# Performance work log

Measured on AMD Instinct MI355X. Metric: run time of the kernel, lower is better.

## Reference

```python
import jax, jax.numpy as jnp
import numpy as np

B, M, N, I, O, NM = 16, 256, 256, 64, 64, 16


def setup_inputs() -> dict:
    key = jax.random.key(0)
    k1, k2, k3, k4, k5 = jax.random.split(key, 5)
    glorot = 1.0 / np.sqrt(I + O)
    return {
        "x": jax.random.normal(k1, (B, M, N, I), dtype=jnp.float32),
        "fw1": jax.random.normal(k2, (I, O, NM, NM, 2), dtype=jnp.float32) * glorot,
        "fw2": jax.random.normal(k3, (I, O, NM, NM, 2), dtype=jnp.float32) * glorot,
        "W": jax.random.normal(k4, (I, O), dtype=jnp.float32) * glorot,
        "b": jnp.zeros((O,), dtype=jnp.float32),
    }


def reference(x, fw1, fw2, W, b):
    # x: [B, M, N, I] -> [B, I, M, N]
    Bs, Ms, Ns, Is = x.shape
    nm = fw1.shape[2]
    xt = jnp.transpose(x, (0, 3, 1, 2))
    # forward rFFT over spatial dims, scaled by 1/sqrt(M*N) as in the TF code
    x_ft = jnp.fft.rfft2(xt, s=(Ms, Ns))  # [B, I, M, N//2+1] complex64
    x_ft = x_ft / jnp.asarray(np.sqrt(Ms * Ns), dtype=x_ft.dtype)
    # complex weights (stack-of-2 real/imag -> complex); complex einsum is
    # exactly the real/imag stacked matmul in the original
    w1 = jax.lax.complex(fw1[..., 0], fw1[..., 1])
    w2 = jax.lax.complex(fw2[..., 0], fw2[..., 1])
    top = jnp.einsum('bixy,ioxy->boxy', x_ft[:, :, :nm, :nm], w1)
    bot = jnp.einsum('bixy,ioxy->boxy', x_ft[:, :, -nm:, :nm], w2)
    mid = jnp.zeros((Bs, top.shape[1], Ms - 2 * nm, nm), dtype=top.dtype)
    out_ft = jnp.concatenate([top, mid, bot], axis=2)          # [B, O, M, nm]
    pad = jnp.zeros((Bs, top.shape[1], Ms, Ms // 2 + 1 - nm), dtype=top.dtype)
    out_ft = jnp.concatenate([out_ft, pad], axis=3)            # [B, O, M, M//2+1]
    y = jnp.fft.irfft2(out_ft, s=(Ns, Ms))                     # [B, O, N, M]
    # TF rescale: sqrt(prod of last two dims of out_ft) = sqrt(N*(M//2+1))
    y = y * jnp.asarray(np.sqrt(Ns * (Ms // 2 + 1)), dtype=y.dtype)
    y = jnp.transpose(y, (0, 2, 3, 1))                         # [B, M, N, O]
    return jax.nn.relu(y @ W + b + y)
```

## Files before the change

### kernel.cpp

```cpp
#include <hip/hip_runtime.h>
#include <hip/hip_bf16.h>


#define PI2F 6.283185307179586f

typedef __attribute__((ext_vector_type(8))) short short8v;
typedef __attribute__((ext_vector_type(4))) float f32x4;

static __device__ __forceinline__ float bf16_to_f(unsigned short h) {
  union { unsigned int u; float f; } v; v.u = ((unsigned int)h) << 16; return v.f;
}
static __device__ __forceinline__ unsigned short f_to_bf16(float f) {
  unsigned int u = __float_as_uint(f);
  u += 0x7fffu + ((u >> 16) & 1u);
  return (unsigned short)(u >> 16);
}

__global__ __launch_bounds__(256) void k_tab(unsigned short* __restrict__ Eg,
                                             unsigned short* __restrict__ CSg) {
  int t = threadIdx.x;
#pragma unroll
  for (int ky = 0; ky < 16; ++ky) {
    int idx = (ky * t) & 255;
    float ss, cc;
    sincosf(PI2F * (float)idx * (1.0f / 256.0f), &ss, &cc);
    Eg[(2 * ky) * 256 + t]     = f_to_bf16(cc);
    Eg[(2 * ky + 1) * 256 + t] = f_to_bf16(-ss);
    CSg[t * 32 + 2 * ky]       = f_to_bf16(cc);
    CSg[t * 32 + 2 * ky + 1]   = f_to_bf16(ss);
  }
}

__global__ __launch_bounds__(256) void k_wt(const float* __restrict__ fw1,
                                            const float* __restrict__ fw2,
                                            float2* __restrict__ wT) {
  int a  = blockIdx.x >> 3;
  int ic = blockIdx.x & 7;
  const float* w = (a < 16) ? fw1 : fw2;
  int xx = a & 15;
#pragma unroll
  for (int k = 0; k < 2; ++k) {
    int p = k * 256 + (int)threadIdx.x;
    int i = ic * 8 + (p >> 6);
    int o = p & 63;
    const float4* s4 = reinterpret_cast<const float4*>(
        w + ((((size_t)i * 64 + o) * 16 + xx) * 16) * 2);
#pragma unroll
    for (int j = 0; j < 8; ++j) {
      float4 q = s4[j];
      wT[(((size_t)(2 * j) * 32 + a) * 64 + i) * 64 + o]     = make_float2(q.x, q.y);
      wT[(((size_t)(2 * j + 1) * 32 + a) * 64 + i) * 64 + o] = make_float2(q.z, q.w);
    }
  }
}

__global__ __launch_bounds__(256) void k1_mfma(const float* __restrict__ x,
                                               const unsigned short* __restrict__ Eg,
                                               float* __restrict__ T) {
  __shared__ unsigned short El[32 * 264];
  int bm = blockIdx.x;
  int b = bm >> 8, m = bm & 255;
  int tid = threadIdx.x;

  {
    const unsigned int* src = reinterpret_cast<const unsigned int*>(Eg);
    unsigned int* dst = reinterpret_cast<unsigned int*>(El);
#pragma unroll
    for (int t = 0; t < 16; ++t) {
      int idx = t * 256 + tid;
      dst[(idx >> 7) * 132 + (idx & 127)] = src[idx];
    }
  }
  __syncthreads();

  int lane = tid & 63, w = tid >> 6;
  int r16 = lane & 15, g4 = lane >> 4;
  const float* xp = x + (size_t)bm * 16384 + (w * 16 + r16);

  f32x4 z = {0.f, 0.f, 0.f, 0.f};
  f32x4 acc0 = z, acc1 = z;

#pragma unroll
  for (int ks = 0; ks < 8; ++ks) {
    int nb = ks * 32 + g4 * 8;
    float xv[8];
#pragma unroll
    for (int j = 0; j < 8; ++j) xv[j] = xp[(size_t)(nb + j) * 64];
    short8v bfr;
#pragma unroll
    for (int j = 0; j < 8; ++j) bfr[j] = (short)f_to_bf16(xv[j]);
    short8v a0 = *reinterpret_cast<const short8v*>(&El[r16 * 264 + nb]);
    short8v a1 = *reinterpret_cast<const short8v*>(&El[(16 + r16) * 264 + nb]);
    acc0 = __builtin_amdgcn_mfma_f32_16x16x32_bf16(a0, bfr, acc0, 0, 0, 0);
    acc1 = __builtin_amdgcn_mfma_f32_16x16x32_bf16(a1, bfr, acc1, 0, 0, 0);
  }

  const float SC = 1.0f / 256.0f;
  int i = w * 16 + r16;
#pragma unroll
  for (int mt = 0; mt < 2; ++mt) {
    f32x4 av = (mt == 0) ? acc0 : acc1;
#pragma unroll
    for (int r = 0; r < 4; ++r) {
      int kc = mt * 16 + g4 * 4 + r;
      int ky = kc >> 1, cmp = kc & 1;
      T[(((size_t)(b * 16 + ky) * 256 + m) * 64 + i) * 2 + cmp] = av[r] * SC;
    }
  }
}

__global__ __launch_bounds__(256) void k2_fwd_m(const float* __restrict__ T,
                                                float* __restrict__ X) {
  int bky = blockIdx.x;
  int ih = threadIdx.x & 15;
  int ag = threadIdx.x >> 4;
  const float* Tp = T + (size_t)bky * 32768 + ih * 8;

  float cd1, sd1n, cd2, sd2n;
  { float ss, cc; sincosf(PI2F * (float)ag * (1.0f / 256.0f), &ss, &cc); cd1 = cc; sd1n = -ss; }
  { float ss, cc; sincosf(PI2F * (float)(ag - 16) * (1.0f / 256.0f), &ss, &cc); cd2 = cc; sd2n = -ss; }
  float c1 = 1.0f, s1 = 0.0f, c2 = 1.0f, s2 = 0.0f;

  float xr1[4], xi1[4], xr2[4], xi2[4];
#pragma unroll
  for (int ii = 0; ii < 4; ++ii) { xr1[ii] = xi1[ii] = xr2[ii] = xi2[ii] = 0.0f; }

#pragma unroll 4
  for (int m = 0; m < 256; ++m) {
    const float4* tp4 = reinterpret_cast<const float4*>(Tp + (size_t)m * 128);
    float4 t0 = tp4[0], t1 = tp4[1];
    float tre[4] = {t0.x, t0.z, t1.x, t1.z};
    float tim[4] = {t0.y, t0.w, t1.y, t1.w};
#pragma unroll
    for (int ii = 0; ii < 4; ++ii) {
      xr1[ii] += tre[ii] * c1 - tim[ii] * s1;
      xi1[ii] += tre[ii] * s1 + tim[ii] * c1;
      xr2[ii] += tre[ii] * c2 - tim[ii] * s2;
      xi2[ii] += tre[ii] * s2 + tim[ii] * c2;
    }
    float cn;
    cn = c1 * cd1 - s1 * sd1n; s1 = c1 * sd1n + s1 * cd1; c1 = cn;
    cn = c2 * cd2 - s2 * sd2n; s2 = c2 * sd2n + s2 * cd2; c2 = cn;
  }

  float* Xp1 = X + ((size_t)bky * 32 + ag) * 128 + ih * 8;
  float* Xp2 = X + ((size_t)bky * 32 + ag + 16) * 128 + ih * 8;
  reinterpret_cast<float4*>(Xp1)[0] = make_float4(xr1[0], xi1[0], xr1[1], xi1[1]);
  reinterpret_cast<float4*>(Xp1)[1] = make_float4(xr1[2], xi1[2], xr1[3], xi1[3]);
  reinterpret_cast<float4*>(Xp2)[0] = make_float4(xr2[0], xi2[0], xr2[1], xi2[1]);
  reinterpret_cast<float4*>(Xp2)[1] = make_float4(xr2[2], xi2[2], xr2[3], xi2[3]);
}

__global__ __launch_bounds__(256) void k3_mix(const float* __restrict__ Xg,
                                              const float* __restrict__ wT,
                                              float* __restrict__ OF) {
  int blk = blockIdx.x;
  int kyy = blk >> 5, a = blk & 31;
  __shared__ float wre[64 * 65];
  __shared__ float wim[64 * 65];
  __shared__ float xsh[16 * 128];

  const float2* wsrc = reinterpret_cast<const float2*>(wT) + (size_t)(kyy * 32 + a) * 4096;
#pragma unroll
  for (int k = 0; k < 16; ++k) {
    int p = k * 256 + (int)threadIdx.x;
    float2 v = wsrc[p];
    int i = p >> 6, o = p & 63;
    wre[i * 65 + o] = v.x;
    wim[i * 65 + o] = v.y;
  }
  {
    int bb = threadIdx.x >> 4, icn = threadIdx.x & 15;
    const float4* xsrc = reinterpret_cast<const float4*>(
        Xg + ((size_t)(bb * 16 + kyy) * 32 + a) * 128);
    float4* xdst = reinterpret_cast<float4*>(xsh + bb * 128);
    xdst[icn * 2]     = xsrc[icn * 2];
    xdst[icn * 2 + 1] = xsrc[icn * 2 + 1];
  }
  __syncthreads();

  int o = threadIdx.x & 63, bg = threadIdx.x >> 6;
#pragma unroll
  for (int bb = 0; bb < 4; ++bb) {
    int b = bg * 4 + bb;
    float ore = 0.0f, oim = 0.0f;
    for (int i = 0; i < 64; ++i) {
      float xr = xsh[b * 128 + 2 * i], xi = xsh[b * 128 + 2 * i + 1];
      float wr = wre[i * 65 + o],     wi = wim[i * 65 + o];
      ore += xr * wr - xi * wi;
      oim += xr * wi + xi * wr;
    }
    reinterpret_cast<float2*>(OF)[(((size_t)b * 16 + kyy) * 32 + a) * 64 + o] =
        make_float2(ore, oim);
  }
}

__global__ __launch_bounds__(256) void k4_inv_kx(const float* __restrict__ OF,
                                                 float* __restrict__ G) {
  int blk = blockIdx.x;
  int b = blk >> 4, ug = blk & 15;
  __shared__ float ofs[16384];
  __shared__ float ct[256], st[256];
  {
    float ssv, ccv;
    sincosf(PI2F * (float)threadIdx.x * (1.0f / 256.0f), &ssv, &ccv);
    ct[threadIdx.x] = ccv;
    st[threadIdx.x] = ssv;
  }
  int o = threadIdx.x & 63, us = threadIdx.x >> 6;
  int u0 = ug * 16 + us * 4;
  const float SC2 = 0.002772904280510622f;

  for (int chunk = 0; chunk < 4; ++chunk) {
    __syncthreads();
    const float4* src = reinterpret_cast<const float4*>(
        OF + (size_t)(b * 16 + chunk * 4) * 4096);
    float4* dst = reinterpret_cast<float4*>(ofs);
#pragma unroll
    for (int k = 0; k < 16; ++k) dst[k * 256 + threadIdx.x] = src[k * 256 + threadIdx.x];
    __syncthreads();

    float accr[4][4], acci[4][4];
#pragma unroll
    for (int du = 0; du < 4; ++du)
#pragma unroll
      for (int kyl = 0; kyl < 4; ++kyl) { accr[du][kyl] = 0.0f; acci[du][kyl] = 0.0f; }

    for (int a = 0; a < 32; ++a) {
      int kx = (a < 16) ? a : (224 + a);
      float ofr[4], ofi[4];
#pragma unroll
      for (int kyl = 0; kyl < 4; ++kyl) {
        ofr[kyl] = ofs[((kyl * 32 + a) * 64 + o) * 2];
        ofi[kyl] = ofs[((kyl * 32 + a) * 64 + o) * 2 + 1];
      }
#pragma unroll
      for (int du = 0; du < 4; ++du) {
        int t = (kx * (u0 + du)) & 255;
        float cv = ct[t], sv = st[t];
#pragma unroll
        for (int kyl = 0; kyl < 4; ++kyl) {
          accr[du][kyl] += ofr[kyl] * cv - ofi[kyl] * sv;
          acci[du][kyl] += ofr[kyl] * sv + ofi[kyl] * cv;
        }
      }
    }
#pragma unroll
    for (int du = 0; du < 4; ++du) {
      int u = u0 + du;
#pragma unroll
      for (int kyl = 0; kyl < 4; ++kyl) {
        int ky = chunk * 4 + kyl;
        float sc = SC2 * ((ky == 0) ? 1.0f : 2.0f);
        reinterpret_cast<float2*>(G)[(((size_t)b * 256 + u) * 16 + ky) * 64 + o] =
            make_float2(accr[du][kyl] * sc, acci[du][kyl] * sc);
      }
    }
  }
}

__global__ __launch_bounds__(256) void k5_mfma(const float* __restrict__ G,
                                               const unsigned short* __restrict__ CSg,
                                               const float* __restrict__ Wg,
                                               const float* __restrict__ bias,
                                               float* __restrict__ out) {
  __shared__ unsigned short csl[256 * 40];
  __shared__ unsigned short gml[64 * 40];
  __shared__ unsigned short yl[256 * 72];
  __shared__ unsigned short wtl[64 * 72];
  __shared__ float bl[64];

  int blk = blockIdx.x;
  int b = blk >> 8, u = blk & 255;
  int tid = threadIdx.x;

  {
    const unsigned int* src = reinterpret_cast<const unsigned int*>(CSg);
    unsigned int* dst = reinterpret_cast<unsigned int*>(csl);
#pragma unroll
    for (int t = 0; t < 16; ++t) {
      int idx = t * 256 + tid;
      dst[(idx >> 4) * 20 + (idx & 15)] = src[idx];
    }
  }
  {
#pragma unroll
    for (int t = 0; t < 16; ++t) {
      int p = t * 256 + tid;
      wtl[(p & 63) * 72 + (p >> 6)] = f_to_bf16(Wg[p]);
    }
  }
  {
    int o = tid & 63, kq = tid >> 6;
    const float2* G2 = reinterpret_cast<const float2*>(G) + ((size_t)blk * 16) * 64;
    unsigned int* gd = reinterpret_cast<unsigned int*>(gml);
#pragma unroll
    for (int q = 0; q < 4; ++q) {
      int ky = kq * 4 + q;
      float2 gv = G2[ky * 64 + o];
      gd[o * 20 + ky] = (unsigned int)f_to_bf16(gv.x) |
                        ((unsigned int)f_to_bf16(-gv.y) << 16);
    }
  }
  if (tid < 64) bl[tid] = bias[tid];
  __syncthreads();

  int lane = tid & 63, w = tid >> 6;
  int r16 = lane & 15, g4 = lane >> 4;
  int kc0 = g4 * 8;

  f32x4 z = {0.f, 0.f, 0.f, 0.f};
  f32x4 acc[4][4];

  short8v af[4], bfx[4];
#pragma unroll
  for (int vt = 0; vt < 4; ++vt)
    af[vt] = *reinterpret_cast<const short8v*>(&csl[(w * 64 + vt * 16 + r16) * 40 + kc0]);
#pragma unroll
  for (int ot = 0; ot < 4; ++ot)
    bfx[ot] = *reinterpret_cast<const short8v*>(&gml[(ot * 16 + r16) * 40 + kc0]);
#pragma unroll
  for (int vt = 0; vt < 4; ++vt)
#pragma unroll
    for (int ot = 0; ot < 4; ++ot)
      acc[vt][ot] = __builtin_amdgcn_mfma_f32_16x16x32_bf16(af[vt], bfx[ot], z, 0, 0, 0);

#pragma unroll
  for (int vt = 0; vt < 4; ++vt)
#pragma unroll
    for (int ot = 0; ot < 4; ++ot)
#pragma unroll
      for (int r = 0; r < 4; ++r)
        yl[(w * 64 + vt * 16 + g4 * 4 + r) * 72 + ot * 16 + r16] = f_to_bf16(acc[vt][ot][r]);
  __syncthreads();

  float bv[4];
#pragma unroll
  for (int ot = 0; ot < 4; ++ot) bv[ot] = bl[ot * 16 + r16];
#pragma unroll
  for (int vt = 0; vt < 4; ++vt)
#pragma unroll
    for (int ot = 0; ot < 4; ++ot)
#pragma unroll
      for (int r = 0; r < 4; ++r) acc[vt][ot][r] += bv[ot];

#pragma unroll
  for (int ks = 0; ks < 2; ++ks) {
    int k0 = ks * 32 + kc0;
    short8v ya[4], wb[4];
#pragma unroll
    for (int vt = 0; vt < 4; ++vt)
      ya[vt] = *reinterpret_cast<const short8v*>(&yl[(w * 64 + vt * 16 + r16) * 72 + k0]);
#pragma unroll
    for (int ot = 0; ot < 4; ++ot)
      wb[ot] = *reinterpret_cast<const short8v*>(&wtl[(ot * 16 + r16) * 72 + k0]);
#pragma unroll
    for (int vt = 0; vt < 4; ++vt)
#pragma unroll
      for (int ot = 0; ot < 4; ++ot)
        acc[vt][ot] = __builtin_amdgcn_mfma_f32_16x16x32_bf16(ya[vt], wb[ot], acc[vt][ot], 0, 0, 0);
  }

  float* ob = out + (size_t)blk * 16384;
#pragma unroll
  for (int vt = 0; vt < 4; ++vt)
#pragma unroll
    for (int r = 0; r < 4; ++r) {
      int v = w * 64 + vt * 16 + g4 * 4 + r;
      float* op = ob + (size_t)v * 64 + r16;
#pragma unroll
      for (int ot = 0; ot < 4; ++ot)
        op[ot * 16] = fmaxf(acc[vt][ot][r], 0.0f);
    }
}

extern "C" void kernel_launch(void* const* d_in, const int* in_sizes, int n_in,
                              void* d_out, int out_size, void* d_ws, size_t ws_size,
                              hipStream_t stream) {
  const float* x   = (const float*)d_in[0];
  const float* fw1 = (const float*)d_in[1];
  const float* fw2 = (const float*)d_in[2];
  const float* W   = (const float*)d_in[3];
  const float* bb  = (const float*)d_in[4];
  float* out = (float*)d_out;

  float* ws = (float*)d_ws;
  float* wT = ws;
  float* T  = ws + 4194304;
  float* X  = ws + 12582912;
  float* OF = ws + 13631488;
  float* G  = T;
  unsigned short* Eg  = (unsigned short*)(ws + 14680064);
  unsigned short* CSg = Eg + 8192;

  hipLaunchKernelGGL(k_tab,    dim3(1),    dim3(256), 0, stream, Eg, CSg);
  hipLaunchKernelGGL(k_wt,     dim3(256),  dim3(256), 0, stream, fw1, fw2, (float2*)wT);
  hipLaunchKernelGGL(k1_mfma,  dim3(4096), dim3(256), 0, stream, x, Eg, T);
  hipLaunchKernelGGL(k2_fwd_m, dim3(256),  dim3(256), 0, stream, T, X);
  hipLaunchKernelGGL(k3_mix,   dim3(512),  dim3(256), 0, stream, X, wT, OF);
  hipLaunchKernelGGL(k4_inv_kx,dim3(256),  dim3(256), 0, stream, OF, G);
  hipLaunchKernelGGL(k5_mfma,  dim3(4096), dim3(256), 0, stream, G, CSg, W, bb, out);
}
```

Measured before the change: 256.6 us.

## Store spectral intermediates in bf16, split DFT stages over more blocks, drop k5 staging

The first-stage output T is now stored as packed bf16 pairs, halving that traffic. The m-direction DFT in k2 is split into four partial chunks, each starting its twiddle at the chunk offset, and k3 sums the partials. k4 is split per ky-chunk across four times as many blocks and writes G already in bf16 MFMA-ready layout. k5 then reads its operands (G, CS table, and a W transpose precomputed in k_tab) directly from global memory instead of staging them in LDS. This exposes more parallelism and cuts bytes moved, at the cost of extra partial-sum traffic and lower-precision intermediates.

After: 241.2 us. -6.0%, faster.

```diff
diff --git a/kernel.cpp b/kernel.cpp
--- a/kernel.cpp
+++ b/kernel.cpp
@@ -15,9 +15,14 @@
   u += 0x7fffu + ((u >> 16) & 1u);
   return (unsigned short)(u >> 16);
 }
+static __device__ __forceinline__ unsigned int pack_bf16(float lo, float hi) {
+  return (unsigned int)f_to_bf16(lo) | ((unsigned int)f_to_bf16(hi) << 16);
+}
 
 __global__ __launch_bounds__(256) void k_tab(unsigned short* __restrict__ Eg,
-                                             unsigned short* __restrict__ CSg) {
+                                             unsigned short* __restrict__ CSg,
+                                             const float* __restrict__ Wg,
+                                             unsigned short* __restrict__ Wtb) {
   int t = threadIdx.x;
 #pragma unroll
   for (int ky = 0; ky < 16; ++ky) {
@@ -29,6 +34,11 @@
     CSg[t * 32 + 2 * ky]       = f_to_bf16(cc);
     CSg[t * 32 + 2 * ky + 1]   = f_to_bf16(ss);
   }
+#pragma unroll
+  for (int k = 0; k < 16; ++k) {
+    int p = k * 256 + t;
+    Wtb[(p & 63) * 64 + (p >> 6)] = f_to_bf16(Wg[p]);
+  }
 }
 
 __global__ __launch_bounds__(256) void k_wt(const float* __restrict__ fw1,
@@ -56,7 +66,7 @@
 
 __global__ __launch_bounds__(256) void k1_mfma(const float* __restrict__ x,
                                                const unsigned short* __restrict__ Eg,
-                                               float* __restrict__ T) {
+                                               unsigned int* __restrict__ Tb) {
   __shared__ unsigned short El[32 * 264];
   int bm = blockIdx.x;
   int b = bm >> 8, m = bm & 255;
@@ -100,37 +110,42 @@
 #pragma unroll
   for (int mt = 0; mt < 2; ++mt) {
     f32x4 av = (mt == 0) ? acc0 : acc1;
-#pragma unroll
-    for (int r = 0; r < 4; ++r) {
-      int kc = mt * 16 + g4 * 4 + r;
-      int ky = kc >> 1, cmp = kc & 1;
-      T[(((size_t)(b * 16 + ky) * 256 + m) * 64 + i) * 2 + cmp] = av[r] * SC;
-    }
-  }
-}
-
-__global__ __launch_bounds__(256) void k2_fwd_m(const float* __restrict__ T,
-                                                float* __restrict__ X) {
-  int bky = blockIdx.x;
+    int ky_a = mt * 8 + g4 * 2;
+    Tb[((size_t)(b * 16 + ky_a) * 256 + m) * 64 + i]       = pack_bf16(av[0] * SC, av[1] * SC);
+    Tb[((size_t)(b * 16 + ky_a + 1) * 256 + m) * 64 + i]   = pack_bf16(av[2] * SC, av[3] * SC);
+  }
+}
+
+__global__ __launch_bounds__(256) void k2_fwd_m(const unsigned int* __restrict__ Tb,
+                                                float* __restrict__ Xp) {
+  int bx = blockIdx.x;
+  int bky = bx & 255, mc = bx >> 8;
+  int m0 = mc * 64;
   int ih = threadIdx.x & 15;
   int ag = threadIdx.x >> 4;
-  const float* Tp = T + (size_t)bky * 32768 + ih * 8;
+  const uint4* Tp4 = reinterpret_cast<const uint4*>(Tb) + (size_t)bky * 4096 + ih;
 
   float cd1, sd1n, cd2, sd2n;
   { float ss, cc; sincosf(PI2F * (float)ag * (1.0f / 256.0f), &ss, &cc); cd1 = cc; sd1n = -ss; }
   { float ss, cc; sincosf(PI2F * (float)(ag - 16) * (1.0f / 256.0f), &ss, &cc); cd2 = cc; sd2n = -ss; }
-  float c1 = 1.0f, s1 = 0.0f, c2 = 1.0f, s2 = 0.0f;
+  float c1, s1, c2, s2;
+  { int t = (ag * m0) & 255; float ss, cc; sincosf(PI2F * (float)t * (1.0f / 256.0f), &ss, &cc); c1 = cc; s1 = -ss; }
+  { int t = ((ag + 240) * m0) & 255; float ss, cc; sincosf(PI2F * (float)t * (1.0f / 256.0f), &ss, &cc); c2 = cc; s2 = -ss; }
 
   float xr1[4], xi1[4], xr2[4], xi2[4];
 #pragma unroll
   for (int ii = 0; ii < 4; ++ii) { xr1[ii] = xi1[ii] = xr2[ii] = xi2[ii] = 0.0f; }
 
 #pragma unroll 4
-  for (int m = 0; m < 256; ++m) {
-    const float4* tp4 = reinterpret_cast<const float4*>(Tp + (size_t)m * 128);
-    float4 t0 = tp4[0], t1 = tp4[1];
-    float tre[4] = {t0.x, t0.z, t1.x, t1.z};
-    float tim[4] = {t0.y, t0.w, t1.y, t1.w};
+  for (int m = 0; m < 64; ++m) {
+    uint4 q = Tp4[(size_t)(m0 + m) * 16];
+    unsigned int dv[4] = {q.x, q.y, q.z, q.w};
+    float tre[4], tim[4];
+#pragma unroll
+    for (int ii = 0; ii < 4; ++ii) {
+      tre[ii] = __uint_as_float(dv[ii] << 16);
+      tim[ii] = __uint_as_float(dv[ii] & 0xffff0000u);
+    }
 #pragma unroll
     for (int ii = 0; ii < 4; ++ii) {
       xr1[ii] += tre[ii] * c1 - tim[ii] * s1;
@@ -143,15 +158,16 @@
     cn = c2 * cd2 - s2 * sd2n; s2 = c2 * sd2n + s2 * cd2; c2 = cn;
   }
 
-  float* Xp1 = X + ((size_t)bky * 32 + ag) * 128 + ih * 8;
-  float* Xp2 = X + ((size_t)bky * 32 + ag + 16) * 128 + ih * 8;
+  float* Xb = Xp + (size_t)mc * 1048576;
+  float* Xp1 = Xb + ((size_t)bky * 32 + ag) * 128 + ih * 8;
+  float* Xp2 = Xb + ((size_t)bky * 32 + ag + 16) * 128 + ih * 8;
   reinterpret_cast<float4*>(Xp1)[0] = make_float4(xr1[0], xi1[0], xr1[1], xi1[1]);
   reinterpret_cast<float4*>(Xp1)[1] = make_float4(xr1[2], xi1[2], xr1[3], xi1[3]);
   reinterpret_cast<float4*>(Xp2)[0] = make_float4(xr2[0], xi2[0], xr2[1], xi2[1]);
   reinterpret_cast<float4*>(Xp2)[1] = make_float4(xr2[2], xi2[2], xr2[3], xi2[3]);
 }
 
-__global__ __launch_bounds__(256) void k3_mix(const float* __restrict__ Xg,
+__global__ __launch_bounds__(256) void k3_mix(const float* __restrict__ Xp,
                                               const float* __restrict__ wT,
                                               float* __restrict__ OF) {
   int blk = blockIdx.x;
@@ -171,11 +187,18 @@
   }
   {
     int bb = threadIdx.x >> 4, icn = threadIdx.x & 15;
-    const float4* xsrc = reinterpret_cast<const float4*>(
-        Xg + ((size_t)(bb * 16 + kyy) * 32 + a) * 128);
+    size_t off = ((size_t)(bb * 16 + kyy) * 32 + a) * 128;
+    float4 a0 = make_float4(0.f, 0.f, 0.f, 0.f), a1 = a0;
+#pragma unroll
+    for (int c = 0; c < 4; ++c) {
+      const float4* xsrc = reinterpret_cast<const float4*>(Xp + (size_t)c * 1048576 + off);
+      float4 q0 = xsrc[icn * 2], q1 = xsrc[icn * 2 + 1];
+      a0.x += q0.x; a0.y += q0.y; a0.z += q0.z; a0.w += q0.w;
+      a1.x += q1.x; a1.y += q1.y; a1.z += q1.z; a1.w += q1.w;
+    }
     float4* xdst = reinterpret_cast<float4*>(xsh + bb * 128);
-    xdst[icn * 2]     = xsrc[icn * 2];
-    xdst[icn * 2 + 1] = xsrc[icn * 2 + 1];
+    xdst[icn * 2]     = a0;
+    xdst[icn * 2 + 1] = a1;
   }
   __syncthreads();
 
@@ -196,9 +219,9 @@
 }
 
 __global__ __launch_bounds__(256) void k4_inv_kx(const float* __restrict__ OF,
-                                                 float* __restrict__ G) {
-  int blk = blockIdx.x;
-  int b = blk >> 4, ug = blk & 15;
+                                                 uint4* __restrict__ Gb4) {
+  int bx = blockIdx.x;
+  int b = bx >> 6, ug = (bx >> 2) & 15, chunk = bx & 3;
   __shared__ float ofs[16384];
   __shared__ float ct[256], st[256];
   {
@@ -207,104 +230,68 @@
     ct[threadIdx.x] = ccv;
     st[threadIdx.x] = ssv;
   }
+  {
+    const float4* src = reinterpret_cast<const float4*>(
+        OF + ((size_t)b * 16 + chunk * 4) * 4096);
+    float4* dst = reinterpret_cast<float4*>(ofs);
+#pragma unroll
+    for (int k = 0; k < 16; ++k) dst[k * 256 + threadIdx.x] = src[k * 256 + threadIdx.x];
+  }
+  __syncthreads();
+
   int o = threadIdx.x & 63, us = threadIdx.x >> 6;
   int u0 = ug * 16 + us * 4;
   const float SC2 = 0.002772904280510622f;
 
-  for (int chunk = 0; chunk < 4; ++chunk) {
-    __syncthreads();
-    const float4* src = reinterpret_cast<const float4*>(
-        OF + (size_t)(b * 16 + chunk * 4) * 4096);
-    float4* dst = reinterpret_cast<float4*>(ofs);
-#pragma unroll
-    for (int k = 0; k < 16; ++k) dst[k * 256 + threadIdx.x] = src[k * 256 + threadIdx.x];
-    __syncthreads();
-
-    float accr[4][4], acci[4][4];
-#pragma unroll
-    for (int du = 0; du < 4; ++du)
-#pragma unroll
-      for (int kyl = 0; kyl < 4; ++kyl) { accr[du][kyl] = 0.0f; acci[du][kyl] = 0.0f; }
-
-    for (int a = 0; a < 32; ++a) {
-      int kx = (a < 16) ? a : (224 + a);
-      float ofr[4], ofi[4];
+  float accr[4][4], acci[4][4];
+#pragma unroll
+  for (int du = 0; du < 4; ++du)
+#pragma unroll
+    for (int kyl = 0; kyl < 4; ++kyl) { accr[du][kyl] = 0.0f; acci[du][kyl] = 0.0f; }
+
+  for (int a = 0; a < 32; ++a) {
+    int kx = (a < 16) ? a : (224 + a);
+    float ofr[4], ofi[4];
+#pragma unroll
+    for (int kyl = 0; kyl < 4; ++kyl) {
+      ofr[kyl] = ofs[((kyl * 32 + a) * 64 + o) * 2];
+      ofi[kyl] = ofs[((kyl * 32 + a) * 64 + o) * 2 + 1];
+    }
+#pragma unroll
+    for (int du = 0; du < 4; ++du) {
+      int t = (kx * (u0 + du)) & 255;
+      float cv = ct[t], sv = st[t];
 #pragma unroll
       for (int kyl = 0; kyl < 4; ++kyl) {
-        ofr[kyl] = ofs[((kyl * 32 + a) * 64 + o) * 2];
-        ofi[kyl] = ofs[((kyl * 32 + a) * 64 + o) * 2 + 1];
+        accr[du][kyl] += ofr[kyl] * cv - ofi[kyl] * sv;
+        acci[du][kyl] += ofr[kyl] * sv + ofi[kyl] * cv;
       }
-#pragma unroll
-      for (int du = 0; du < 4; ++du) {
-        int t = (kx * (u0 + du)) & 255;
-        float cv = ct[t], sv = st[t];
-#pragma unroll
-        for (int kyl = 0; kyl < 4; ++kyl) {
-          accr[du][kyl] += ofr[kyl] * cv - ofi[kyl] * sv;
-          acci[du][kyl] += ofr[kyl] * sv + ofi[kyl] * cv;
-        }
-      }
-    }
-#pragma unroll
-    for (int du = 0; du < 4; ++du) {
-      int u = u0 + du;
-#pragma unroll
-      for (int kyl = 0; kyl < 4; ++kyl) {
-        int ky = chunk * 4 + kyl;
-        float sc = SC2 * ((ky == 0) ? 1.0f : 2.0f);
-        reinterpret_cast<float2*>(G)[(((size_t)b * 256 + u) * 16 + ky) * 64 + o] =
-            make_float2(accr[du][kyl] * sc, acci[du][kyl] * sc);
-      }
-    }
-  }
-}
-
-__global__ __launch_bounds__(256) void k5_mfma(const float* __restrict__ G,
+    }
+  }
+#pragma unroll
+  for (int du = 0; du < 4; ++du) {
+    int u = u0 + du;
+    unsigned int wv[4];
+#pragma unroll
+    for (int kyl = 0; kyl < 4; ++kyl) {
+      int ky = chunk * 4 + kyl;
+      float sc = SC2 * ((ky == 0) ? 1.0f : 2.0f);
+      wv[kyl] = pack_bf16(accr[du][kyl] * sc, -acci[du][kyl] * sc);
+    }
+    uint4 pk; pk.x = wv[0]; pk.y = wv[1]; pk.z = wv[2]; pk.w = wv[3];
+    Gb4[(((size_t)b * 256 + u) * 64 + o) * 4 + chunk] = pk;
+  }
+}
+
+__global__ __launch_bounds__(256) void k5_mfma(const unsigned short* __restrict__ Gb,
                                                const unsigned short* __restrict__ CSg,
-                                               const float* __restrict__ Wg,
+                                               const unsigned short* __restrict__ Wtb,
                                                const float* __restrict__ bias,
                                                float* __restrict__ out) {
-  __shared__ unsigned short csl[256 * 40];
-  __shared__ unsigned short gml[64 * 40];
   __shared__ unsigned short yl[256 * 72];
-  __shared__ unsigned short wtl[64 * 72];
-  __shared__ float bl[64];
 
   int blk = blockIdx.x;
-  int b = blk >> 8, u = blk & 255;
   int tid = threadIdx.x;
-
-  {
-    const unsigned int* src = reinterpret_cast<const unsigned int*>(CSg);
-    unsigned int* dst = reinterpret_cast<unsigned int*>(csl);
-#pragma unroll
-    for (int t = 0; t < 16; ++t) {
-      int idx = t * 256 + tid;
-      dst[(idx >> 4) * 20 + (idx & 15)] = src[idx];
-    }
-  }
-  {
-#pragma unroll
-    for (int t = 0; t < 16; ++t) {
-      int p = t * 256 + tid;
-      wtl[(p & 63) * 72 + (p >> 6)] = f_to_bf16(Wg[p]);
-    }
-  }
-  {
-    int o = tid & 63, kq = tid >> 6;
-    const float2* G2 = reinterpret_cast<const float2*>(G) + ((size_t)blk * 16) * 64;
-    unsigned int* gd = reinterpret_cast<unsigned int*>(gml);
-#pragma unroll
-    for (int q = 0; q < 4; ++q) {
-      int ky = kq * 4 + q;
-      float2 gv = G2[ky * 64 + o];
-      gd[o * 20 + ky] = (unsigned int)f_to_bf16(gv.x) |
-                        ((unsigned int)f_to_bf16(-gv.y) << 16);
-    }
-  }
-  if (tid < 64) bl[tid] = bias[tid];
-  __syncthreads();
-
   int lane = tid & 63, w = tid >> 6;
   int r16 = lane & 15, g4 = lane >> 4;
   int kc0 = g4 * 8;
@@ -315,10 +302,11 @@
   short8v af[4], bfx[4];
 #pragma unroll
   for (int vt = 0; vt < 4; ++vt)
-    af[vt] = *reinterpret_cast<const short8v*>(&csl[(w * 64 + vt * 16 + r16) * 40 + kc0]);
+    af[vt] = *reinterpret_cast<const short8v*>(&CSg[(w * 64 + vt * 16 + r16) * 32 + kc0]);
 #pragma unroll
   for (int ot = 0; ot < 4; ++ot)
-    bfx[ot] = *reinterpret_cast<const short8v*>(&gml[(ot * 16 + r16) * 40 + kc0]);
+    bfx[ot] = *reinterpret_cast<const short8v*>(
+        &Gb[((size_t)blk * 64 + ot * 16 + r16) * 32 + kc0]);
 #pragma unroll
   for (int vt = 0; vt < 4; ++vt)
 #pragma unroll
@@ -334,15 +322,14 @@
         yl[(w * 64 + vt * 16 + g4 * 4 + r) * 72 + ot * 16 + r16] = f_to_bf16(acc[vt][ot][r]);
   __syncthreads();
 
-  float bv[4];
-#pragma unroll
-  for (int ot = 0; ot < 4; ++ot) bv[ot] = bl[ot * 16 + r16];
-#pragma unroll
-  for (int vt = 0; vt < 4; ++vt)
-#pragma unroll
-    for (int ot = 0; ot < 4; ++ot)
-#pragma unroll
-      for (int r = 0; r < 4; ++r) acc[vt][ot][r] += bv[ot];
+#pragma unroll
+  for (int ot = 0; ot < 4; ++ot) {
+    float bv = bias[ot * 16 + r16];
+#pragma unroll
+    for (int vt = 0; vt < 4; ++vt)
+#pragma unroll
+      for (int r = 0; r < 4; ++r) acc[vt][ot][r] += bv;
+  }
 
 #pragma unroll
   for (int ks = 0; ks < 2; ++ks) {
@@ -353,7 +340,7 @@
       ya[vt] = *reinterpret_cast<const short8v*>(&yl[(w * 64 + vt * 16 + r16) * 72 + k0]);
 #pragma unroll
     for (int ot = 0; ot < 4; ++ot)
-      wb[ot] = *reinterpret_cast<const short8v*>(&wtl[(ot * 16 + r16) * 72 + k0]);
+      wb[ot] = *reinterpret_cast<const short8v*>(&Wtb[(ot * 16 + r16) * 64 + k0]);
 #pragma unroll
     for (int vt = 0; vt < 4; ++vt)
 #pragma unroll
@@ -385,19 +372,21 @@
   float* out = (float*)d_out;
 
   float* ws = (float*)d_ws;
-  float* wT = ws;
-  float* T  = ws + 4194304;
-  float* X  = ws + 12582912;
-  float* OF = ws + 13631488;
-  float* G  = T;
-  unsigned short* Eg  = (unsigned short*)(ws + 14680064);
+  float* wT          = ws;
+  unsigned int* Tb   = (unsigned int*)(ws + 4194304);
+  float* Xp          = ws + 8388608;
+  float* OF          = ws + 12582912;
+  unsigned int* Gb   = (unsigned int*)(ws + 13631488);
+  unsigned short* Eg  = (unsigned short*)(ws + 17825792);
   unsigned short* CSg = Eg + 8192;
-
-  hipLaunchKernelGGL(k_tab,    dim3(1),    dim3(256), 0, stream, Eg, CSg);
+  unsigned short* Wtb = CSg + 8192;
+
+  hipLaunchKernelGGL(k_tab,    dim3(1),    dim3(256), 0, stream, Eg, CSg, W, Wtb);
   hipLaunchKernelGGL(k_wt,     dim3(256),  dim3(256), 0, stream, fw1, fw2, (float2*)wT);
-  hipLaunchKernelGGL(k1_mfma,  dim3(4096), dim3(256), 0, stream, x, Eg, T);
-  hipLaunchKernelGGL(k2_fwd_m, dim3(256),  dim3(256), 0, stream, T, X);
-  hipLaunchKernelGGL(k3_mix,   dim3(512),  dim3(256), 0, stream, X, wT, OF);
-  hipLaunchKernelGGL(k4_inv_kx,dim3(256),  dim3(256), 0, stream, OF, G);
-  hipLaunchKernelGGL(k5_mfma,  dim3(4096), dim3(256), 0, stream, G, CSg, W, bb, out);
-}
+  hipLaunchKernelGGL(k1_mfma,  dim3(4096), dim3(256), 0, stream, x, Eg, Tb);
+  hipLaunchKernelGGL(k2_fwd_m, dim3(1024), dim3(256), 0, stream, Tb, Xp);
+  hipLaunchKernelGGL(k3_mix,   dim3(512),  dim3(256), 0, stream, Xp, wT, OF);
+  hipLaunchKernelGGL(k4_inv_kx,dim3(1024), dim3(256), 0, stream, OF, (uint4*)Gb);
+  hipLaunchKernelGGL(k5_mfma,  dim3(4096), dim3(256), 0, stream,
+                     (const unsigned short*)Gb, CSg, Wtb, bb, out);
+}
```
